# Optimization experiments

Measured on AMD Instinct MI355X. Metric: run time of the kernel, lower is better.

## Reference

```python
import jax, jax.numpy as jnp
import numpy as np

B, I, H, O = 16384, 512, 1024, 512

def setup_inputs() -> dict:
    key = jax.random.key(0)
    ks = jax.random.split(key, 8)
    s_x = 1.0 / np.sqrt(I)
    s_h = 1.0 / np.sqrt(H)
    inp = jax.random.normal(ks[0], (B, I), jnp.float32)
    h = jax.random.normal(ks[1], (B, H), jnp.float32)
    c = jax.random.normal(ks[2], (B, H), jnp.float32)
    # stacked gate weights, order [i, o, f, z]
    Wx = jax.random.uniform(ks[3], (4, H, I), jnp.float32, -s_x, s_x)
    Wh = jax.random.uniform(ks[4], (4, H, H), jnp.float32, -s_h, s_h)
    # z-gate h2z weight is re-initialized with standard normal in reset_parameters
    Wh = Wh.at[3].set(jax.random.normal(ks[5], (H, H), jnp.float32))
    # biases per module init: i=linspace(-1,-10), o=0, f=linspace(1,10), z=0
    bx = jnp.stack([
        jnp.linspace(-1.0, -10.0, H, dtype=jnp.float32),
        jnp.zeros((H,), jnp.float32),
        jnp.linspace(1.0, 10.0, H, dtype=jnp.float32),
        jnp.zeros((H,), jnp.float32),
    ])
    Wout = jax.random.uniform(ks[6], (O, H), jnp.float32, -s_h, s_h)
    bout = jax.random.uniform(ks[7], (O,), jnp.float32, -s_h, s_h)
    return {"inp": inp, "h": h, "c": c, "Wx": Wx, "bx": bx, "Wh": Wh,
            "Wout": Wout, "bout": bout}

def reference(inp, h, c, Wx, bx, Wh, Wout, bout):
    # fused gate pre-activations: two stacked GEMMs
    # gx: [4, B, H], gh: [4, B, H]
    gx = jnp.einsum('bi,ghi->gbh', inp, Wx) + bx[:, None, :]
    gh = jnp.einsum('bh,gkh->gbk', h, Wh)
    g = gx + gh
    i = jax.nn.sigmoid(g[0])
    o = jax.nn.sigmoid(g[1])
    f = jax.nn.sigmoid(g[2])
    z = jnp.tanh(g[3])
    c_new = i * z + f * c
    h_new = o * jnp.tanh(c_new)  # act_fn = tanh
    out = h_new @ Wout.T + bout
    return (out, h_new)
```

## Files before the change

### kernel.cpp

```cpp
#include <hip/hip_runtime.h>
#include <stdint.h>

#define BB 16384
#define II 512
#define HH 1024
#define OO 512

typedef short s16x8 __attribute__((ext_vector_type(8)));
typedef float f32x4 __attribute__((ext_vector_type(4)));

__device__ __forceinline__ unsigned short f2bf(float x) {
  union { float f; unsigned u; } v; v.f = x;
  return (unsigned short)((v.u + 0x7fffu + ((v.u >> 16) & 1u)) >> 16);
}
__device__ __forceinline__ float bf2f(unsigned short b) {
  union { unsigned u; float f; } v; v.u = ((unsigned)b) << 16;
  return v.f;
}
__device__ __forceinline__ float sigmoid_f(float x) {
  return 1.0f / (1.0f + __expf(-x));
}
__device__ __forceinline__ float tanh_f(float x) {
  float ax = fabsf(x);
  float e = __expf(-2.0f * ax);
  float t = (1.0f - e) / (1.0f + e);
  return x >= 0.0f ? t : -t;
}

__device__ __forceinline__ void stage16(const void* g, void* l) {
  __builtin_amdgcn_global_load_lds((const __attribute__((address_space(1))) void*)g,
                                   (__attribute__((address_space(3))) void*)l,
                                   16, 0, 0);
}

__device__ __forceinline__ void mma_step64(const unsigned short* As, const unsigned short* Bs,
                                           f32x4 acc[4][4], int lane, int wave) {
  const int wm = wave & 1, wn = wave >> 1;
  const int ln = lane & 15, q = lane >> 4;
#pragma unroll
  for (int s = 0; s < 2; ++s) {
    s16x8 af[4], bfr[4];
#pragma unroll
    for (int i = 0; i < 4; ++i) {
      const int r = wm * 64 + i * 16 + ln;
      af[i] = *(const s16x8*)(As + r * 64 + ((((s << 2) + q) + r) & 7) * 8);
    }
#pragma unroll
    for (int i = 0; i < 4; ++i) {
      const int r = wn * 64 + i * 16 + ln;
      bfr[i] = *(const s16x8*)(Bs + r * 64 + ((((s << 2) + q) + r) & 7) * 8);
    }
#pragma unroll
    for (int mi = 0; mi < 4; ++mi)
#pragma unroll
      for (int ni = 0; ni < 4; ++ni)
        acc[mi][ni] = __builtin_amdgcn_mfma_f32_16x16x32_bf16(af[mi], bfr[ni], acc[mi][ni], 0, 0, 0);
  }
}

__global__ __launch_bounds__(256) void prep_all(const float* __restrict__ inp,
                                                const float* __restrict__ h,
                                                const float* __restrict__ Wx,
                                                const float* __restrict__ Wh,
                                                const float* __restrict__ Wout,
                                                unsigned short* __restrict__ Xb,
                                                unsigned short* __restrict__ Hlo,
                                                unsigned short* __restrict__ Wg,
                                                unsigned short* __restrict__ Wz2,
                                                unsigned short* __restrict__ Wo) {
  const int bid = blockIdx.x;
  if (bid < 12288) {
    int t = bid * 256 + threadIdx.x;
    int base = t * 8;
    int b = base / 1536;
    int k = base - b * 1536;
    const float* src = (k < 512) ? (inp + b * 512 + k) : (h + b * 1024 + (k - 512));
    float4 v0 = *(const float4*)src;
    float4 v1 = *(const float4*)(src + 4);
    float f[8] = {v0.x, v0.y, v0.z, v0.w, v1.x, v1.y, v1.z, v1.w};
    unsigned short hi[8];
#pragma unroll
    for (int i = 0; i < 8; ++i) hi[i] = f2bf(f[i]);
    *(s16x8*)(Xb + base) = *(s16x8*)hi;
    if (k >= 512) {
      unsigned short lo[8];
#pragma unroll
      for (int i = 0; i < 8; ++i) lo[i] = f2bf(f[i] - bf2f(hi[i]));
      *(s16x8*)(Hlo + b * 1024 + (k - 512)) = *(s16x8*)lo;
    }
  } else if (bid < 15360) {
    int t = (bid - 12288) * 256 + threadIdx.x;
    int base = t * 8;
    int n = base / 1536;
    int k = base - n * 1536;
    int r = n & 255;
    int gate = (r >> 4) & 3;
    int unit = ((n >> 8) << 6) + (((r >> 6) & 3) << 4) + (r & 15);
    const float* src = (k < 512) ? (Wx + (gate * 1024 + unit) * 512 + k)
                                 : (Wh + (gate * 1024 + unit) * 1024 + (k - 512));
    float4 v0 = *(const float4*)src;
    float4 v1 = *(const float4*)(src + 4);
    float f[8] = {v0.x, v0.y, v0.z, v0.w, v1.x, v1.y, v1.z, v1.w};
    unsigned short o[8];
#pragma unroll
    for (int i = 0; i < 8; ++i) o[i] = f2bf(f[i]);
    *(s16x8*)(Wg + base) = *(s16x8*)o;
  } else if (bid < 16384) {
    const float* Whz = Wh + 3 * 1024 * 1024;
    int t = (bid - 15360) * 256 + threadIdx.x;
    int base = t * 8;
    int n = base >> 11;
    int k = base & 2047;
    int klo = (k < 1024) ? k : (k - 1024);
    const float* src = Whz + n * 1024 + klo;
    float4 v0 = *(const float4*)src;
    float4 v1 = *(const float4*)(src + 4);
    float f[8] = {v0.x, v0.y, v0.z, v0.w, v1.x, v1.y, v1.z, v1.w};
    unsigned short o[8];
    if (k < 1024) {
#pragma unroll
      for (int i = 0; i < 8; ++i) { unsigned short h_ = f2bf(f[i]); o[i] = f2bf(f[i] - bf2f(h_)); }
    } else {
#pragma unroll
      for (int i = 0; i < 8; ++i) o[i] = f2bf(f[i]);
    }
    *(s16x8*)(Wz2 + base) = *(s16x8*)o;
  } else {
    int t = (bid - 16384) * 256 + threadIdx.x;
    int base = t * 8;
    float4 v0 = *(const float4*)(Wout + base);
    float4 v1 = *(const float4*)(Wout + base + 4);
    float f[8] = {v0.x, v0.y, v0.z, v0.w, v1.x, v1.y, v1.z, v1.w};
    unsigned short o[8];
#pragma unroll
    for (int i = 0; i < 8; ++i) o[i] = f2bf(f[i]);
    *(s16x8*)(Wo + base) = *(s16x8*)o;
  }
}


#define RD_A(CA, MI, KS) (*(const s16x8*)((CA) + ((KS) ? aoff1 : aoff0) + (MI) * 1024))
#define RD_B(CB, NI, KS) (*(const s16x8*)((CB) + ((KS) ? boff1 : boff0) + (NI) * 1024))
#define VM8 asm volatile("s_waitcnt vmcnt(8)" ::: "memory")
#define VM4 asm volatile("s_waitcnt vmcnt(4)" ::: "memory")
#define VM0 asm volatile("s_waitcnt vmcnt(0)" ::: "memory")
#define LGKM8 asm volatile("s_waitcnt lgkmcnt(8)" ::: "memory")
#define LGKM0 asm volatile("s_waitcnt lgkmcnt(0)" ::: "memory")
#define SB0 __builtin_amdgcn_sched_barrier(0)
#define BARR __builtin_amdgcn_s_barrier()
#define VMNONE ((void)0)
#define NOST ((void)0)

#define AQ(S, CA, Q) do { \
  S[0] = RD_A(CA, 2 * (Q), 0);  S[1] = RD_A(CA, 2 * (Q) + 1, 0); \
  S[2] = RD_A(CA, 2 * (Q), 1);  S[3] = RD_A(CA, 2 * (Q) + 1, 1); } while (0)
#define BH(BQ, CB, KS) do { \
  BQ[4 * (KS) + 0] = RD_B(CB, 0, KS); BQ[4 * (KS) + 1] = RD_B(CB, 1, KS); \
  BQ[4 * (KS) + 2] = RD_B(CB, 2, KS); BQ[4 * (KS) + 3] = RD_B(CB, 3, KS); } while (0)

#define SA_H0(TT, DB) do { \
  stage16(gA[0][0] + (size_t)(TT) * 64, (DB)); \
  stage16(gA[0][1] + (size_t)(TT) * 64, (DB) + 4096); } while (0)
#define SA_H1(TT, DB) do { \
  stage16(gA[1][0] + (size_t)(TT) * 64, (DB) + 8192); \
  stage16(gA[1][1] + (size_t)(TT) * 64, (DB) + 12288); } while (0)
#define SB_H0(TT, DB) do { \
  stage16(gB[0][0] + (size_t)(TT) * 64, (DB)); \
  stage16(gB[0][1] + (size_t)(TT) * 64, (DB) + 4096); } while (0)
#define SB_H1(TT, DB) do { \
  stage16(gB[1][0] + (size_t)(TT) * 64, (DB) + 8192); \
  stage16(gB[1][1] + (size_t)(TT) * 64, (DB) + 12288); } while (0)
#define ZSA_H0(TT, DB) do { \
  const unsigned short *z0_, *z1_; \
  if ((TT) < 16) { z0_ = gAX[0][0] + (size_t)(TT) * 64; z1_ = gAX[0][1] + (size_t)(TT) * 64; } \
  else { z0_ = gAH[0][0] + (size_t)((TT) - 16) * 64; z1_ = gAH[0][1] + (size_t)((TT) - 16) * 64; } \
  stage16(z0_, (DB)); stage16(z1_, (DB) + 4096); } while (0)
#define ZSA_H1(TT, DB) do { \
  const unsigned short *z2_, *z3_; \
  if ((TT) < 16) { z2_ = gAX[1][0] + (size_t)(TT) * 64; z3_ = gAX[1][1] + (size_t)(TT) * 64; } \
  else { z2_ = gAH[1][0] + (size_t)((TT) - 16) * 64; z3_ = gAH[1][1] + (size_t)((TT) - 16) * 64; } \
  stage16(z2_, (DB) + 8192); stage16(z3_, (DB) + 12288); } while (0)

#define MFMAQ(Q, S) do { \
  __builtin_amdgcn_s_setprio(1); \
  _Pragma("unroll") \
  for (int ni = 0; ni < 4; ++ni) { \
    acc[2 * (Q)    ][ni] = __builtin_amdgcn_mfma_f32_16x16x32_bf16(S[0], bq[ni], acc[2 * (Q)    ][ni], 0, 0, 0); \
    acc[2 * (Q) + 1][ni] = __builtin_amdgcn_mfma_f32_16x16x32_bf16(S[1], bq[ni], acc[2 * (Q) + 1][ni], 0, 0, 0); \
  } \
  _Pragma("unroll") \
  for (int ni = 0; ni < 4; ++ni) { \
    acc[2 * (Q)    ][ni] = __builtin_amdgcn_mfma_f32_16x16x32_bf16(S[2], bq[4 + ni], acc[2 * (Q)    ][ni], 0, 0, 0); \
    acc[2 * (Q) + 1][ni] = __builtin_amdgcn_mfma_f32_16x16x32_bf16(S[3], bq[4 + ni], acc[2 * (Q) + 1][ni], 0, 0, 0); \
  } \
  __builtin_amdgcn_s_setprio(0); \
} while (0)

#define KTILE(CA, CB, S0, S1, S2, S3, VMX) do { \
  s16x8 bq[8], aE[4], aO[4]; \
  BH(bq, CB, 0); BH(bq, CB, 1); \
  AQ(aE, CA, 0); \
  S0; \
  LGKM8; \
  BARR; LGKM0; SB0; \
  MFMAQ(0, aE); \
  BARR; \
  AQ(aO, CA, 1); S1; \
  BARR; LGKM0; SB0; \
  MFMAQ(1, aO); \
  BARR; \
  AQ(aE, CA, 2); S2; \
  BARR; LGKM0; SB0; \
  MFMAQ(2, aE); \
  BARR; \
  AQ(aO, CA, 3); S3; \
  BARR; LGKM0; SB0; \
  MFMAQ(3, aO); \
  VMX; BARR; \
} while (0)

__global__ __launch_bounds__(512, 2) void gemm_gates2(const unsigned short* __restrict__ Xb,
                                                      const unsigned short* __restrict__ Wg,
                                                      const float* __restrict__ bx,
                                                      const float* __restrict__ cold,
                                                      const unsigned short* __restrict__ Dgz,
                                                      float* __restrict__ hnew,
                                                      unsigned short* __restrict__ hnewb) {
  __shared__ unsigned short lds[2][2][16384];
  const int tid = threadIdx.x;
  const int lane = tid & 63, wave = tid >> 6;
  const int wm = wave & 1, wn = wave >> 1;
  const int ln = lane & 15, qlane = lane >> 4;
  const int n0 = blockIdx.x << 8, m0 = blockIdx.y << 8;
  const int sr = tid >> 3;
  const int j = ((tid & 7) - (sr & 7)) & 7;

  const unsigned short* gA[2][2];
  const unsigned short* gB[2][2];
#pragma unroll
  for (int hh = 0; hh < 2; ++hh)
#pragma unroll
    for (int u = 0; u < 2; ++u) {
      const int row = hh * 128 + u * 64 + sr;
      gA[hh][u] = Xb + (size_t)(m0 + row) * 1536 + j * 8;
      gB[hh][u] = Wg + (size_t)(n0 + row) * 1536 + j * 8;
    }
  unsigned short* const dA0 = &lds[0][0][0] + (tid & ~63) * 8;
  unsigned short* const dB0 = &lds[0][1][0] + (tid & ~63) * 8;
  unsigned short* const dA1 = &lds[1][0][0] + (tid & ~63) * 8;
  unsigned short* const dB1 = &lds[1][1][0] + (tid & ~63) * 8;
  const unsigned short* const lA0 = &lds[0][0][0];
  const unsigned short* const lB0 = &lds[0][1][0];
  const unsigned short* const lA1 = &lds[1][0][0];
  const unsigned short* const lB1 = &lds[1][1][0];
  const int sl0 = ((qlane + ln) & 7) * 8;
  const int sl1 = sl0 ^ 32;
  const int aoff0 = (wm * 128 + ln) * 64 + sl0;
  const int aoff1 = (wm * 128 + ln) * 64 + sl1;
  const int boff0 = (wn * 64 + ln) * 64 + sl0;
  const int boff1 = (wn * 64 + ln) * 64 + sl1;

  f32x4 acc[8][4] = {};

  SA_H0(0, dA0); SA_H1(0, dA0); SB_H0(0, dB0); SB_H1(0, dB0);
  SA_H0(1, dA1); SA_H1(1, dA1); SB_H0(1, dB1); SB_H1(1, dB1);
  VM8;
  BARR;

  KTILE(lA0, lB0, NOST, NOST, SB_H0(2, dB0), SB_H1(2, dB0), VM4);
#pragma unroll 1
  for (int t = 1; t < 21; t += 2) {
    KTILE(lA1, lB1, SA_H0(t + 1, dA0), SA_H1(t + 1, dA0),
                    SB_H0(t + 2, dB1), SB_H1(t + 2, dB1), VM4);
    KTILE(lA0, lB0, SA_H0(t + 2, dA1), SA_H1(t + 2, dA1),
                    SB_H0(t + 3, dB0), SB_H1(t + 3, dB0), VM4);
  }
  KTILE(lA1, lB1, SA_H0(22, dA0), SA_H1(22, dA0),
                  SB_H0(23, dB1), SB_H1(23, dB1), VM4);
  KTILE(lA0, lB0, SA_H0(23, dA1), SA_H1(23, dA1), NOST, NOST, VM0);
  KTILE(lA1, lB1, NOST, NOST, NOST, NOST, VMNONE);

  const int unit = ((int)blockIdx.x << 6) + (wn << 4) + ln;
  const float bi = bx[unit];
  const float bo = bx[1024 + unit];
  const float bfg = bx[2048 + unit];
  const float bz = bx[3072 + unit];
#pragma unroll
  for (int mi = 0; mi < 8; ++mi) {
#pragma unroll
    for (int r = 0; r < 4; ++r) {
      const int b = m0 + wm * 128 + mi * 16 + qlane * 4 + r;
      const int idx = b * 1024 + unit;
      const float gi = acc[mi][0][r] + bi;
      const float go = acc[mi][1][r] + bo;
      const float gf = acc[mi][2][r] + bfg;
      const float gz = acc[mi][3][r] + bz + bf2f(Dgz[idx]);
      const float iv = sigmoid_f(gi);
      const float ov = sigmoid_f(go);
      const float fv = sigmoid_f(gf);
      const float zv = tanh_f(gz);
      const float cn = iv * zv + fv * cold[idx];
      const float hn = ov * tanh_f(cn);
      hnew[idx] = hn;
      hnewb[idx] = f2bf(hn);
    }
  }
}

__global__ __launch_bounds__(512, 2) void gemm_zcorr2(const unsigned short* __restrict__ Xb,
                                                      const unsigned short* __restrict__ Hlo,
                                                      const unsigned short* __restrict__ Wz2,
                                                      unsigned short* __restrict__ Dgz) {
  __shared__ unsigned short lds[2][2][16384];
  const int tid = threadIdx.x;
  const int lane = tid & 63, wave = tid >> 6;
  const int wm = wave & 1, wn = wave >> 1;
  const int ln = lane & 15, qlane = lane >> 4;
  const int n0 = blockIdx.x << 8, m0 = blockIdx.y << 8;
  const int sr = tid >> 3;
  const int j = ((tid & 7) - (sr & 7)) & 7;

  const unsigned short* gAX[2][2];
  const unsigned short* gAH[2][2];
  const unsigned short* gB[2][2];
#pragma unroll
  for (int hh = 0; hh < 2; ++hh)
#pragma unroll
    for (int u = 0; u < 2; ++u) {
      const int row = hh * 128 + u * 64 + sr;
      gAX[hh][u] = Xb  + (size_t)(m0 + row) * 1536 + 512 + j * 8;
      gAH[hh][u] = Hlo + (size_t)(m0 + row) * 1024 + j * 8;
      gB[hh][u]  = Wz2 + (size_t)(n0 + row) * 2048 + j * 8;
    }
  unsigned short* const dA0 = &lds[0][0][0] + (tid & ~63) * 8;
  unsigned short* const dB0 = &lds[0][1][0] + (tid & ~63) * 8;
  unsigned short* const dA1 = &lds[1][0][0] + (tid & ~63) * 8;
  unsigned short* const dB1 = &lds[1][1][0] + (tid & ~63) * 8;
  const unsigned short* const lA0 = &lds[0][0][0];
  const unsigned short* const lB0 = &lds[0][1][0];
  const unsigned short* const lA1 = &lds[1][0][0];
  const unsigned short* const lB1 = &lds[1][1][0];
  const int sl0 = ((qlane + ln) & 7) * 8;
  const int sl1 = sl0 ^ 32;
  const int aoff0 = (wm * 128 + ln) * 64 + sl0;
  const int aoff1 = (wm * 128 + ln) * 64 + sl1;
  const int boff0 = (wn * 64 + ln) * 64 + sl0;
  const int boff1 = (wn * 64 + ln) * 64 + sl1;

  f32x4 acc[8][4] = {};

  ZSA_H0(0, dA0); ZSA_H1(0, dA0); SB_H0(0, dB0); SB_H1(0, dB0);
  ZSA_H0(1, dA1); ZSA_H1(1, dA1); SB_H0(1, dB1); SB_H1(1, dB1);
  VM8;
  BARR;

  KTILE(lA0, lB0, NOST, NOST, SB_H0(2, dB0), SB_H1(2, dB0), VM4);
#pragma unroll 1
  for (int t = 1; t < 29; t += 2) {
    KTILE(lA1, lB1, ZSA_H0(t + 1, dA0), ZSA_H1(t + 1, dA0),
                    SB_H0(t + 2, dB1), SB_H1(t + 2, dB1), VM4);
    KTILE(lA0, lB0, ZSA_H0(t + 2, dA1), ZSA_H1(t + 2, dA1),
                    SB_H0(t + 3, dB0), SB_H1(t + 3, dB0), VM4);
  }
  KTILE(lA1, lB1, ZSA_H0(30, dA0), ZSA_H1(30, dA0),
                  SB_H0(31, dB1), SB_H1(31, dB1), VM4);
  KTILE(lA0, lB0, ZSA_H0(31, dA1), ZSA_H1(31, dA1), NOST, NOST, VM0);
  KTILE(lA1, lB1, NOST, NOST, NOST, NOST, VMNONE);

#pragma unroll
  for (int mi = 0; mi < 8; ++mi) {
#pragma unroll
    for (int r = 0; r < 4; ++r) {
      const int b = m0 + wm * 128 + mi * 16 + qlane * 4 + r;
#pragma unroll
      for (int ni = 0; ni < 4; ++ni) {
        const int n = n0 + wn * 64 + ni * 16 + ln;
        Dgz[b * 1024 + n] = f2bf(acc[mi][ni][r]);
      }
    }
  }
}

__global__ __launch_bounds__(256) void gemm_out(const unsigned short* __restrict__ Hb,
                                                const unsigned short* __restrict__ Wo,
                                                const float* __restrict__ bout,
                                                float* __restrict__ out) {
  __shared__ unsigned short As[8192];
  __shared__ unsigned short Bs[8192];
  const int n0 = blockIdx.x * 128;
  const int m0 = blockIdx.y * 128;
  const int tid = threadIdx.x, lane = tid & 63, wave = tid >> 6;
  const unsigned short *ga[4], *gb[4];
  unsigned short *la[4], *lb[4];
#pragma unroll
  for (int u = 0; u < 4; ++u) {
    int p = u * 256 + tid;
    int r = p >> 3;
    int jj = ((p & 7) - r) & 7;
    ga[u] = Hb + (size_t)(m0 + r) * 1024 + jj * 8;
    gb[u] = Wo + (size_t)(n0 + r) * 1024 + jj * 8;
    la[u] = As + (u * 256 + (tid & ~63)) * 8;
    lb[u] = Bs + (u * 256 + (tid & ~63)) * 8;
  }
  f32x4 acc[4][4] = {};
  for (int kk = 0; kk < 16; ++kk) {
#pragma unroll
    for (int u = 0; u < 4; ++u) { stage16(ga[u], la[u]); stage16(gb[u], lb[u]); }
#pragma unroll
    for (int u = 0; u < 4; ++u) { ga[u] += 64; gb[u] += 64; }
    __syncthreads();
    mma_step64(As, Bs, acc, lane, wave);
    __syncthreads();
  }
  const int wm = wave & 1, wn = wave >> 1;
  const int ln = lane & 15, q = lane >> 4;
  float bo_[4];
#pragma unroll
  for (int ni = 0; ni < 4; ++ni) bo_[ni] = bout[n0 + wn * 64 + ni * 16 + ln];
#pragma unroll
  for (int mi = 0; mi < 4; ++mi) {
#pragma unroll
    for (int r = 0; r < 4; ++r) {
      const int b = m0 + wm * 64 + mi * 16 + q * 4 + r;
#pragma unroll
      for (int ni = 0; ni < 4; ++ni) {
        const int n = n0 + wn * 64 + ni * 16 + ln;
        out[b * 512 + n] = acc[mi][ni][r] + bo_[ni];
      }
    }
  }
}

extern "C" void kernel_launch(void* const* d_in, const int* in_sizes, int n_in,
                              void* d_out, int out_size, void* d_ws, size_t ws_size,
                              hipStream_t stream) {
  const float* inp  = (const float*)d_in[0];
  const float* h    = (const float*)d_in[1];
  const float* c    = (const float*)d_in[2];
  const float* Wx   = (const float*)d_in[3];
  const float* bx   = (const float*)d_in[4];
  const float* Wh   = (const float*)d_in[5];
  const float* Wout = (const float*)d_in[6];
  const float* bout = (const float*)d_in[7];

  float* out  = (float*)d_out;
  float* hnew = out + (size_t)BB * OO;

  char* ws = (char*)d_ws;
  unsigned short* Xb  = (unsigned short*)(ws);
  unsigned short* Wg  = (unsigned short*)(ws + 50331648);
  unsigned short* Wo  = (unsigned short*)(ws + 62914560);
  unsigned short* Hb  = (unsigned short*)(ws + 63963136);
  unsigned short* Hlo = (unsigned short*)(ws + 97517568);
  unsigned short* Wz2 = (unsigned short*)(ws + 131072000);
  unsigned short* Dgz = (unsigned short*)(ws + 135266304);

  prep_all<<<16640, 256, 0, stream>>>(inp, h, Wx, Wh, Wout, Xb, Hlo, Wg, Wz2, Wo);
  gemm_zcorr2<<<dim3(4, 64),  512, 0, stream>>>(Xb, Hlo, Wz2, Dgz);
  gemm_gates2<<<dim3(16, 64), 512, 0, stream>>>(Xb, Wg, bx, c, Dgz, hnew, Hb);
  gemm_out  <<<dim3(4, 128),  256, 0, stream>>>(Hb, Wo, bout, out);
}
```

Before: 551.8 us.

## Load B operand directly from global into registers, drop B LDS staging

After: 730.0 us. +32.3%, slower.

```diff
diff --git a/kernel.cpp b/kernel.cpp
--- a/kernel.cpp
+++ b/kernel.cpp
@@ -139,24 +139,30 @@
 }
 
 
-#define RD_A(CA, MI, KS) (*(const s16x8*)((CA) + ((KS) ? aoff1 : aoff0) + (MI) * 1024))
-#define RD_B(CB, NI, KS) (*(const s16x8*)((CB) + ((KS) ? boff1 : boff0) + (NI) * 1024))
 #define VM8 asm volatile("s_waitcnt vmcnt(8)" ::: "memory")
-#define VM4 asm volatile("s_waitcnt vmcnt(4)" ::: "memory")
+#define VM2 asm volatile("s_waitcnt vmcnt(2)" ::: "memory")
 #define VM0 asm volatile("s_waitcnt vmcnt(0)" ::: "memory")
-#define LGKM8 asm volatile("s_waitcnt lgkmcnt(8)" ::: "memory")
 #define LGKM0 asm volatile("s_waitcnt lgkmcnt(0)" ::: "memory")
 #define SB0 __builtin_amdgcn_sched_barrier(0)
 #define BARR __builtin_amdgcn_s_barrier()
 #define VMNONE ((void)0)
 #define NOST ((void)0)
-
+#define NOBAR ((void)0)
+
+#define RD_A(CA, MI, KS) (*(const s16x8*)((CA) + ((KS) ? aoff1 : aoff0) + (MI) * 1024))
 #define AQ(S, CA, Q) do { \
   S[0] = RD_A(CA, 2 * (Q), 0);  S[1] = RD_A(CA, 2 * (Q) + 1, 0); \
   S[2] = RD_A(CA, 2 * (Q), 1);  S[3] = RD_A(CA, 2 * (Q) + 1, 1); } while (0)
-#define BH(BQ, CB, KS) do { \
-  BQ[4 * (KS) + 0] = RD_B(CB, 0, KS); BQ[4 * (KS) + 1] = RD_B(CB, 1, KS); \
-  BQ[4 * (KS) + 2] = RD_B(CB, 2, KS); BQ[4 * (KS) + 3] = RD_B(CB, 3, KS); } while (0)
+
+#define GBL(P) (*(const __attribute__((address_space(1))) s16x8*)(P))
+#define BLOAD_CUR do { \
+  bq[0] = GBL(gBv0);      bq[1] = GBL(gBv1);      bq[2] = GBL(gBv2);      bq[3] = GBL(gBv3); \
+  bq[4] = GBL(gBv0 + 32); bq[5] = GBL(gBv1 + 32); bq[6] = GBL(gBv2 + 32); bq[7] = GBL(gBv3 + 32); \
+} while (0)
+#define BLOAD_NEXT do { \
+  gBv0 += 64; gBv1 += 64; gBv2 += 64; gBv3 += 64; \
+  BLOAD_CUR; \
+} while (0)
 
 #define SA_H0(TT, DB) do { \
   stage16(gA[0][0] + (size_t)(TT) * 64, (DB)); \
@@ -164,12 +170,6 @@
 #define SA_H1(TT, DB) do { \
   stage16(gA[1][0] + (size_t)(TT) * 64, (DB) + 8192); \
   stage16(gA[1][1] + (size_t)(TT) * 64, (DB) + 12288); } while (0)
-#define SB_H0(TT, DB) do { \
-  stage16(gB[0][0] + (size_t)(TT) * 64, (DB)); \
-  stage16(gB[0][1] + (size_t)(TT) * 64, (DB) + 4096); } while (0)
-#define SB_H1(TT, DB) do { \
-  stage16(gB[1][0] + (size_t)(TT) * 64, (DB) + 8192); \
-  stage16(gB[1][1] + (size_t)(TT) * 64, (DB) + 12288); } while (0)
 #define ZSA_H0(TT, DB) do { \
   const unsigned short *z0_, *z1_; \
   if ((TT) < 16) { z0_ = gAX[0][0] + (size_t)(TT) * 64; z1_ = gAX[0][1] + (size_t)(TT) * 64; } \
@@ -196,27 +196,20 @@
   __builtin_amdgcn_s_setprio(0); \
 } while (0)
 
-#define KTILE(CA, CB, S0, S1, S2, S3, VMX) do { \
-  s16x8 bq[8], aE[4], aO[4]; \
-  BH(bq, CB, 0); BH(bq, CB, 1); \
-  AQ(aE, CA, 0); \
-  S0; \
-  LGKM8; \
-  BARR; LGKM0; SB0; \
+#define KTILE(CA, S0, S1, VMB, BL3, VME, EBAR) do { \
+  AQ(aE, CA, 0); S0; \
+  BARR; VMB; LGKM0; SB0; \
   MFMAQ(0, aE); \
-  BARR; \
   AQ(aO, CA, 1); S1; \
   BARR; LGKM0; SB0; \
   MFMAQ(1, aO); \
-  BARR; \
-  AQ(aE, CA, 2); S2; \
+  AQ(aE, CA, 2); \
   BARR; LGKM0; SB0; \
   MFMAQ(2, aE); \
-  BARR; \
-  AQ(aO, CA, 3); S3; \
+  AQ(aO, CA, 3); \
   BARR; LGKM0; SB0; \
   MFMAQ(3, aO); \
-  VMX; BARR; \
+  BL3; VME; EBAR; \
 } while (0)
 
 __global__ __launch_bounds__(512, 2) void gemm_gates2(const unsigned short* __restrict__ Xb,
@@ -226,7 +219,7 @@
                                                       const unsigned short* __restrict__ Dgz,
                                                       float* __restrict__ hnew,
                                                       unsigned short* __restrict__ hnewb) {
-  __shared__ unsigned short lds[2][2][16384];
+  __shared__ unsigned short lds[2][16384];
   const int tid = threadIdx.x;
   const int lane = tid & 63, wave = tid >> 6;
   const int wm = wave & 1, wn = wave >> 1;
@@ -236,49 +229,44 @@
   const int j = ((tid & 7) - (sr & 7)) & 7;
 
   const unsigned short* gA[2][2];
-  const unsigned short* gB[2][2];
 #pragma unroll
   for (int hh = 0; hh < 2; ++hh)
 #pragma unroll
     for (int u = 0; u < 2; ++u) {
       const int row = hh * 128 + u * 64 + sr;
       gA[hh][u] = Xb + (size_t)(m0 + row) * 1536 + j * 8;
-      gB[hh][u] = Wg + (size_t)(n0 + row) * 1536 + j * 8;
-    }
-  unsigned short* const dA0 = &lds[0][0][0] + (tid & ~63) * 8;
-  unsigned short* const dB0 = &lds[0][1][0] + (tid & ~63) * 8;
-  unsigned short* const dA1 = &lds[1][0][0] + (tid & ~63) * 8;
-  unsigned short* const dB1 = &lds[1][1][0] + (tid & ~63) * 8;
-  const unsigned short* const lA0 = &lds[0][0][0];
-  const unsigned short* const lB0 = &lds[0][1][0];
-  const unsigned short* const lA1 = &lds[1][0][0];
-  const unsigned short* const lB1 = &lds[1][1][0];
+    }
+  const unsigned short* gBv0 = Wg + (size_t)(n0 + wn * 64 +  0 + ln) * 1536 + qlane * 8;
+  const unsigned short* gBv1 = Wg + (size_t)(n0 + wn * 64 + 16 + ln) * 1536 + qlane * 8;
+  const unsigned short* gBv2 = Wg + (size_t)(n0 + wn * 64 + 32 + ln) * 1536 + qlane * 8;
+  const unsigned short* gBv3 = Wg + (size_t)(n0 + wn * 64 + 48 + ln) * 1536 + qlane * 8;
+
+  unsigned short* const dA0 = &lds[0][0] + (tid & ~63) * 8;
+  unsigned short* const dA1 = &lds[1][0] + (tid & ~63) * 8;
+  const unsigned short* const lA0 = &lds[0][0];
+  const unsigned short* const lA1 = &lds[1][0];
   const int sl0 = ((qlane + ln) & 7) * 8;
   const int sl1 = sl0 ^ 32;
   const int aoff0 = (wm * 128 + ln) * 64 + sl0;
   const int aoff1 = (wm * 128 + ln) * 64 + sl1;
-  const int boff0 = (wn * 64 + ln) * 64 + sl0;
-  const int boff1 = (wn * 64 + ln) * 64 + sl1;
 
   f32x4 acc[8][4] = {};
-
-  SA_H0(0, dA0); SA_H1(0, dA0); SB_H0(0, dB0); SB_H1(0, dB0);
-  SA_H0(1, dA1); SA_H1(1, dA1); SB_H0(1, dB1); SB_H1(1, dB1);
+  s16x8 bq[8], aE[4], aO[4];
+
+  SA_H0(0, dA0); SA_H1(0, dA0);
+  BLOAD_CUR;
   VM8;
   BARR;
 
-  KTILE(lA0, lB0, NOST, NOST, SB_H0(2, dB0), SB_H1(2, dB0), VM4);
+  KTILE(lA0, SA_H0(1, dA1), SA_H1(1, dA1), VM2, BLOAD_NEXT, VM8, BARR);
 #pragma unroll 1
   for (int t = 1; t < 21; t += 2) {
-    KTILE(lA1, lB1, SA_H0(t + 1, dA0), SA_H1(t + 1, dA0),
-                    SB_H0(t + 2, dB1), SB_H1(t + 2, dB1), VM4);
-    KTILE(lA0, lB0, SA_H0(t + 2, dA1), SA_H1(t + 2, dA1),
-                    SB_H0(t + 3, dB0), SB_H1(t + 3, dB0), VM4);
-  }
-  KTILE(lA1, lB1, SA_H0(22, dA0), SA_H1(22, dA0),
-                  SB_H0(23, dB1), SB_H1(23, dB1), VM4);
-  KTILE(lA0, lB0, SA_H0(23, dA1), SA_H1(23, dA1), NOST, NOST, VM0);
-  KTILE(lA1, lB1, NOST, NOST, NOST, NOST, VMNONE);
+    KTILE(lA1, SA_H0(t + 1, dA0), SA_H1(t + 1, dA0), VM2, BLOAD_NEXT, VM8, BARR);
+    KTILE(lA0, SA_H0(t + 2, dA1), SA_H1(t + 2, dA1), VM2, BLOAD_NEXT, VM8, BARR);
+  }
+  KTILE(lA1, SA_H0(22, dA0), SA_H1(22, dA0), VM2, BLOAD_NEXT, VM8, BARR);
+  KTILE(lA0, SA_H0(23, dA1), SA_H1(23, dA1), VM2, BLOAD_NEXT, VM8, BARR);
+  KTILE(lA1, NOST, NOST, VM0, NOST, VMNONE, NOBAR);
 
   const int unit = ((int)blockIdx.x << 6) + (wn << 4) + ln;
   const float bi = bx[unit];
@@ -311,7 +299,7 @@
                                                       const unsigned short* __restrict__ Hlo,
                                                       const unsigned short* __restrict__ Wz2,
                                                       unsigned short* __restrict__ Dgz) {
-  __shared__ unsigned short lds[2][2][16384];
+  __shared__ unsigned short lds[2][16384];
   const int tid = threadIdx.x;
   const int lane = tid & 63, wave = tid >> 6;
   const int wm = wave & 1, wn = wave >> 1;
@@ -322,7 +310,6 @@
 
   const unsigned short* gAX[2][2];
   const unsigned short* gAH[2][2];
-  const unsigned short* gB[2][2];
 #pragma unroll
   for (int hh = 0; hh < 2; ++hh)
 #pragma unroll
@@ -330,42 +317,38 @@
       const int row = hh * 128 + u * 64 + sr;
       gAX[hh][u] = Xb  + (size_t)(m0 + row) * 1536 + 512 + j * 8;
       gAH[hh][u] = Hlo + (size_t)(m0 + row) * 1024 + j * 8;
-      gB[hh][u]  = Wz2 + (size_t)(n0 + row) * 2048 + j * 8;
-    }
-  unsigned short* const dA0 = &lds[0][0][0] + (tid & ~63) * 8;
-  unsigned short* const dB0 = &lds[0][1][0] + (tid & ~63) * 8;
-  unsigned short* const dA1 = &lds[1][0][0] + (tid & ~63) * 8;
-  unsigned short* const dB1 = &lds[1][1][0] + (tid & ~63) * 8;
-  const unsigned short* const lA0 = &lds[0][0][0];
-  const unsigned short* const lB0 = &lds[0][1][0];
-  const unsigned short* const lA1 = &lds[1][0][0];
-  const unsigned short* const lB1 = &lds[1][1][0];
+    }
+  const unsigned short* gBv0 = Wz2 + (size_t)(n0 + wn * 64 +  0 + ln) * 2048 + qlane * 8;
+  const unsigned short* gBv1 = Wz2 + (size_t)(n0 + wn * 64 + 16 + ln) * 2048 + qlane * 8;
+  const unsigned short* gBv2 = Wz2 + (size_t)(n0 + wn * 64 + 32 + ln) * 2048 + qlane * 8;
+  const unsigned short* gBv3 = Wz2 + (size_t)(n0 + wn * 64 + 48 + ln) * 2048 + qlane * 8;
+
+  unsigned short* const dA0 = &lds[0][0] + (tid & ~63) * 8;
+  unsigned short* const dA1 = &lds[1][0] + (tid & ~63) * 8;
+  const unsigned short* const lA0 = &lds[0][0];
+  const unsigned short* const lA1 = &lds[1][0];
   const int sl0 = ((qlane + ln) & 7) * 8;
   const int sl1 = sl0 ^ 32;
   const int aoff0 = (wm * 128 + ln) * 64 + sl0;
   const int aoff1 = (wm * 128 + ln) * 64 + sl1;
-  const int boff0 = (wn * 64 + ln) * 64 + sl0;
-  const int boff1 = (wn * 64 + ln) * 64 + sl1;
 
   f32x4 acc[8][4] = {};
-
-  ZSA_H0(0, dA0); ZSA_H1(0, dA0); SB_H0(0, dB0); SB_H1(0, dB0);
-  ZSA_H0(1, dA1); ZSA_H1(1, dA1); SB_H0(1, dB1); SB_H1(1, dB1);
+  s16x8 bq[8], aE[4], aO[4];
+
+  ZSA_H0(0, dA0); ZSA_H1(0, dA0);
+  BLOAD_CUR;
   VM8;
   BARR;
 
-  KTILE(lA0, lB0, NOST, NOST, SB_H0(2, dB0), SB_H1(2, dB0), VM4);
+  KTILE(lA0, ZSA_H0(1, dA1), ZSA_H1(1, dA1), VM2, BLOAD_NEXT, VM8, BARR);
 #pragma unroll 1
   for (int t = 1; t < 29; t += 2) {
-    KTILE(lA1, lB1, ZSA_H0(t + 1, dA0), ZSA_H1(t + 1, dA0),
-                    SB_H0(t + 2, dB1), SB_H1(t + 2, dB1), VM4);
-    KTILE(lA0, lB0, ZSA_H0(t + 2, dA1), ZSA_H1(t + 2, dA1),
-                    SB_H0(t + 3, dB0), SB_H1(t + 3, dB0), VM4);
-  }
-  KTILE(lA1, lB1, ZSA_H0(30, dA0), ZSA_H1(30, dA0),
-                  SB_H0(31, dB1), SB_H1(31, dB1), VM4);
-  KTILE(lA0, lB0, ZSA_H0(31, dA1), ZSA_H1(31, dA1), NOST, NOST, VM0);
-  KTILE(lA1, lB1, NOST, NOST, NOST, NOST, VMNONE);
+    KTILE(lA1, ZSA_H0(t + 1, dA0), ZSA_H1(t + 1, dA0), VM2, BLOAD_NEXT, VM8, BARR);
+    KTILE(lA0, ZSA_H0(t + 2, dA1), ZSA_H1(t + 2, dA1), VM2, BLOAD_NEXT, VM8, BARR);
+  }
+  KTILE(lA1, ZSA_H0(30, dA0), ZSA_H1(30, dA0), VM2, BLOAD_NEXT, VM8, BARR);
+  KTILE(lA0, ZSA_H0(31, dA1), ZSA_H1(31, dA1), VM2, BLOAD_NEXT, VM8, BARR);
+  KTILE(lA1, NOST, NOST, VM0, NOST, VMNONE, NOBAR);
 
 #pragma unroll
   for (int mi = 0; mi < 8; ++mi) {
```
